# Kernel tuning notes

Measured on AMD Instinct MI355X. Metric: run time of the kernel, lower is better.

The kernel has to match this reference:

```python
import jax, jax.numpy as jnp
import numpy as np
import math

ALPHA = 1.0
EPS = 1e-8
PI = math.pi


def setup_inputs() -> dict:
    key = jax.random.key(0)
    k1, k2 = jax.random.split(key)
    B, L, P = 32, 8, 1024
    pred_keypoints = jax.random.normal(k1, (B, L, P, 2), dtype=jnp.float32)
    gt_keypoints = jax.random.normal(k2, (B, L, P, 2), dtype=jnp.float32)
    return {"pred_keypoints": pred_keypoints, "gt_keypoints": gt_keypoints}


def _segments(pts):
    """pts: [..., P, 2] -> (dl [..., S, 2], mid [..., S, 2]) with S = P-1.
    Faithful to torch: tangent = diff/sqrt(|diff|^2+eps), dl = tangent*|diff| (norm w/o eps)."""
    diff = pts[..., 1:, :] - pts[..., :-1, :]
    sumsq = jnp.sum(diff * diff, axis=-1)
    seg_len = jnp.sqrt(sumsq)                       # torch.norm(p2-p1)
    scale = seg_len / jnp.sqrt(sumsq + EPS)          # |dl| factor vs raw diff
    dl = diff * scale[..., None]
    mid = 0.5 * (pts[..., 1:, :] + pts[..., :-1, :])
    return dl, mid


def _self_energy(dl, mid):
    """dl, mid: [B, L, S, 2] -> per-lane self energy [B, L]."""
    S = dl.shape[-2]
    line = jnp.sum(jnp.linalg.norm(dl, axis=-1), axis=-1) / (8.0 * PI)
    dots = jnp.einsum('blid,bljd->blij', dl, dl)                 # [B,L,S,S]
    r = jnp.linalg.norm(mid[..., None, :, :] - mid[..., :, None, :], axis=-1) + EPS
    mask = jnp.triu(jnp.ones((S, S), dtype=bool), k=1)           # i < j pairs only
    pair = jnp.sum(jnp.where(mask, dots / (8.0 * PI * r), 0.0), axis=(-1, -2))
    return line + pair


def _interaction_energy(dl_p, mid_p, dl_g, mid_g):
    """-> per-lane interaction energy [B, L] (note dot(dl1, -dl2) in torch)."""
    dots = jnp.einsum('blid,bljd->blij', dl_p, dl_g)             # [B,L,Sp,Sg]
    r = jnp.linalg.norm(mid_g[..., None, :, :] - mid_p[..., :, None, :], axis=-1) + EPS
    return jnp.sum(-dots / (4.0 * PI * r), axis=(-1, -2))


def reference(pred_keypoints, gt_keypoints):
    B = pred_keypoints.shape[0]
    dl_p, mid_p = _segments(pred_keypoints)
    dl_g, mid_g = _segments(gt_keypoints)
    e_self_p = _self_energy(dl_p, mid_p)
    e_self_g = _self_energy(dl_g, mid_g)
    e_int = _interaction_energy(dl_p, mid_p, dl_g, mid_g)
    lane_loss = e_self_p + e_self_g - 2.0 * ALPHA * e_int        # [B, L]
    return jnp.sum(lane_loss) / B
```

## Files before the change

kernel.cpp:

```cpp
#include <hip/hip_runtime.h>
#include <math.h>

constexpr int B = 32;
constexpr int P = 1024;
constexpr int S = 1023;
constexpr float EPS = 1e-8f;

#define INV8PI 0.039788735772973836
#define INV2PI 0.15915494309189535

typedef float f32x4 __attribute__((ext_vector_type(4)));

__device__ const unsigned char UMT[36] = {
    0,0,0,0,0,0,0,0,0,0,
    1,1,1,1,1,1,1,1,1,1,
    2,2,2,2,2,2,2,2,2,2,2,2,2,2,2,2};
__device__ const unsigned char URB[36] = {
    0,0,0,0,1,1,1,2,2,3,
    0,0,0,0,1,1,1,2,2,3,
    0,0,0,0,1,1,1,1,2,2,2,2,3,3,3,3};
__device__ const unsigned char UCB[36] = {
    0,1,2,3,1,2,3,2,3,3,
    0,1,2,3,1,2,3,2,3,3,
    0,1,2,3,0,1,2,3,0,1,2,3,0,1,2,3};

__device__ __forceinline__ float4 make_seg(const float2* __restrict__ pts, int i) {
    float2 a = pts[i];
    float2 b = pts[i + 1];
    float dx = b.x - a.x, dy = b.y - a.y;
    float s2 = dx * dx + dy * dy;
    float scale = sqrtf(s2) / sqrtf(s2 + EPS);
    float4 r;
    r.x = dx * scale;
    r.y = dy * scale;
    r.z = 0.5f * (a.x + b.x);
    r.w = 0.5f * (a.y + b.y);
    return r;
}

__global__ __launch_bounds__(256, 4) void
pair_kernel(const float* __restrict__ pred, const float* __restrict__ gt,
            double* __restrict__ acc) {
    __shared__ float sA[2][4][1024];
    __shared__ double wsum[8];

    const int lane = blockIdx.y;
    const int ublk = blockIdx.x;
    const int tid  = threadIdx.x;
    const int wv   = tid >> 6;
    const int l    = tid & 63;

    const float2* pp = (const float2*)pred + (size_t)lane * P;
    const float2* pg = (const float2*)gt   + (size_t)lane * P;

    for (int j = tid; j < S; j += 256) {
        float4 s = make_seg(pp, j);
        sA[0][0][j] = s.x; sA[0][1][j] = s.y; sA[0][2][j] = s.z; sA[0][3][j] = s.w;
        float4 t = make_seg(pg, j);
        sA[1][0][j] = t.x; sA[1][1][j] = t.y; sA[1][2][j] = t.z; sA[1][3][j] = t.w;
    }
    if (tid == 0) {
        sA[0][0][S] = 0.f; sA[0][1][S] = 0.f; sA[0][2][S] = 0.f; sA[0][3][S] = 0.f;
        sA[1][0][S] = 0.f; sA[1][1][S] = 0.f; sA[1][2][S] = 0.f; sA[1][3][S] = 0.f;
    }
    __syncthreads();

    double acc_self = 0.0, acc_int = 0.0;

    if (ublk == 0) {
        float lf = 0.f;
        for (int j = tid; j < S; j += 256) {
            lf += sqrtf(sA[0][0][j] * sA[0][0][j] + sA[0][1][j] * sA[0][1][j]);
            lf += sqrtf(sA[1][0][j] * sA[1][0][j] + sA[1][1][j] * sA[1][1][j]);
        }
        acc_self += (double)lf;
    }

    for (int t = 0; t < 3; ++t) {
        const int u  = 12 * ublk + wv + 4 * t;
        const int mt = UMT[u], rb = URB[u], cb = UCB[u];
        const int rm = (mt == 1) ? 1 : 0;
        const int cm = (mt == 0) ? 0 : 1;

        const int rq = rb * 64 + l;
        f32x4 rx4 = ((const f32x4*)sA[rm][0])[rq];
        f32x4 ry4 = ((const f32x4*)sA[rm][1])[rq];
        f32x4 ru4 = ((const f32x4*)sA[rm][2])[rq];
        f32x4 rv4 = ((const f32x4*)sA[rm][3])[rq];
        const float rx[4] = {rx4.x, rx4.y, rx4.z, rx4.w};
        const float ry[4] = {ry4.x, ry4.y, ry4.z, ry4.w};
        const float ru[4] = {ru4.x, ru4.y, ru4.z, ru4.w};
        const float rv[4] = {rv4.x, rv4.y, rv4.z, rv4.w};

        const f32x4* qx = (const f32x4*)sA[cm][0];
        const f32x4* qy = (const f32x4*)sA[cm][1];
        const f32x4* qu = (const f32x4*)sA[cm][2];
        const f32x4* qv = (const f32x4*)sA[cm][3];

        f32x4 a[4] = {{0,0,0,0},{0,0,0,0},{0,0,0,0},{0,0,0,0}};
        const int q0 = cb * 64;
        const int i0 = rb * 256 + 4 * l;
        const bool masked = (mt < 2) && (rb == cb);

        if (!masked) {
#pragma unroll 2
            for (int q = q0; q < q0 + 64; ++q) {
                f32x4 cx = qx[q], cy = qy[q], cu = qu[q], cv = qv[q];
#pragma unroll
                for (int k = 0; k < 4; ++k) {
                    f32x4 rdx = cu - ru[k];
                    f32x4 rdy = cv - rv[k];
                    f32x4 d2  = rdx * rdx + (rdy * rdy + (f32x4)1e-30f);
                    f32x4 dot = rx[k] * cx + ry[k] * cy;
                    f32x4 rs;
                    rs.x = __builtin_amdgcn_rsqf(d2.x);
                    rs.y = __builtin_amdgcn_rsqf(d2.y);
                    rs.z = __builtin_amdgcn_rsqf(d2.z);
                    rs.w = __builtin_amdgcn_rsqf(d2.w);
                    a[k] += dot * rs;
                }
            }
        } else {
#pragma unroll 2
            for (int q = q0; q < q0 + 64; ++q) {
                f32x4 cx = qx[q], cy = qy[q], cu = qu[q], cv = qv[q];
                const int jb = 4 * q;
#pragma unroll
                for (int k = 0; k < 4; ++k) {
                    f32x4 rdx = cu - ru[k];
                    f32x4 rdy = cv - rv[k];
                    f32x4 d2  = rdx * rdx + (rdy * rdy + (f32x4)1e-30f);
                    f32x4 dot = rx[k] * cx + ry[k] * cy;
                    f32x4 rs;
                    rs.x = __builtin_amdgcn_rsqf(d2.x);
                    rs.y = __builtin_amdgcn_rsqf(d2.y);
                    rs.z = __builtin_amdgcn_rsqf(d2.z);
                    rs.w = __builtin_amdgcn_rsqf(d2.w);
                    f32x4 tv = dot * rs;
                    const int ik = i0 + k;
                    tv.x = (jb + 0 > ik) ? tv.x : 0.f;
                    tv.y = (jb + 1 > ik) ? tv.y : 0.f;
                    tv.z = (jb + 2 > ik) ? tv.z : 0.f;
                    tv.w = (jb + 3 > ik) ? tv.w : 0.f;
                    a[k] += tv;
                }
            }
        }

        double su = 0.0;
#pragma unroll
        for (int k = 0; k < 4; ++k)
            su += (double)a[k].x + (double)a[k].y + (double)a[k].z + (double)a[k].w;
        if (mt == 2) acc_int += su; else acc_self += su;
    }

    for (int off = 32; off; off >>= 1) {
        acc_self += __shfl_down(acc_self, off, 64);
        acc_int  += __shfl_down(acc_int,  off, 64);
    }
    if (l == 0) { wsum[wv] = acc_self; wsum[4 + wv] = acc_int; }
    __syncthreads();
    if (tid == 0) {
        double ts = wsum[0] + wsum[1] + wsum[2] + wsum[3];
        double ti = wsum[4] + wsum[5] + wsum[6] + wsum[7];
        atomicAdd(acc, ts * INV8PI + ti * INV2PI);
    }
}

__global__ void finalize_kernel(const double* __restrict__ acc, float* __restrict__ out) {
    out[0] = (float)(acc[0] / (double)B);
}

extern "C" void kernel_launch(void* const* d_in, const int* in_sizes, int n_in,
                              void* d_out, int out_size, void* d_ws, size_t ws_size,
                              hipStream_t stream) {
    const float* pred = (const float*)d_in[0];
    const float* gt   = (const float*)d_in[1];
    double* acc = (double*)d_ws;

    hipMemsetAsync(d_ws, 0, sizeof(double), stream);

    dim3 grid(3, 256);
    pair_kernel<<<grid, dim3(256), 0, stream>>>(pred, gt, acc);
    finalize_kernel<<<1, 1, 0, stream>>>(acc, (float*)d_out);
}
```

Baseline: 188.2 us.

## Split pair work into per-wave 256x32 panels across a much larger grid

Replaces the 3-block-per-lane schedule, where each wave processed three 256x256 tiles from a fully staged LDS copy, with a 72-block-per-lane grid. Each wave now handles one 256x32 panel and builds its own row and column segments from global memory. This aims to raise occupancy and load balance and to shrink wasted work on diagonal tiles. In exchange, segments are recomputed redundantly and the number of global double atomics grows greatly.

```diff
diff --git a/kernel.cpp b/kernel.cpp
--- a/kernel.cpp
+++ b/kernel.cpp
@@ -10,19 +10,6 @@
 #define INV2PI 0.15915494309189535
 
 typedef float f32x4 __attribute__((ext_vector_type(4)));
-
-__device__ const unsigned char UMT[36] = {
-    0,0,0,0,0,0,0,0,0,0,
-    1,1,1,1,1,1,1,1,1,1,
-    2,2,2,2,2,2,2,2,2,2,2,2,2,2,2,2};
-__device__ const unsigned char URB[36] = {
-    0,0,0,0,1,1,1,2,2,3,
-    0,0,0,0,1,1,1,2,2,3,
-    0,0,0,0,1,1,1,1,2,2,2,2,3,3,3,3};
-__device__ const unsigned char UCB[36] = {
-    0,1,2,3,1,2,3,2,3,3,
-    0,1,2,3,1,2,3,2,3,3,
-    0,1,2,3,0,1,2,3,0,1,2,3,0,1,2,3};
 
 __device__ __forceinline__ float4 make_seg(const float2* __restrict__ pts, int i) {
     float2 a = pts[i];
@@ -38,133 +25,121 @@
     return r;
 }
 
-__global__ __launch_bounds__(256, 4) void
+__global__ __launch_bounds__(256, 8) void
 pair_kernel(const float* __restrict__ pred, const float* __restrict__ gt,
             double* __restrict__ acc) {
-    __shared__ float sA[2][4][1024];
-    __shared__ double wsum[8];
+    __shared__ __align__(16) float pan[4][4][32];
+    __shared__ double wsum[4];
 
-    const int lane = blockIdx.y;
-    const int ublk = blockIdx.x;
-    const int tid  = threadIdx.x;
-    const int wv   = tid >> 6;
-    const int l    = tid & 63;
+    const int plane = blockIdx.y;
+    const int tid   = threadIdx.x;
+    const int wv    = tid >> 6;
+    const int l     = tid & 63;
+    const int s     = blockIdx.x * 4 + wv;
 
-    const float2* pp = (const float2*)pred + (size_t)lane * P;
-    const float2* pg = (const float2*)gt   + (size_t)lane * P;
+    int mt, rb, cs;
+    if (s < 160) {
+        mt = (s < 80) ? 0 : 1;
+        const int u = (s < 80) ? s : s - 80;
+        if      (u < 32) { rb = 0; cs = u; }
+        else if (u < 56) { rb = 1; cs = u - 32 + 8; }
+        else if (u < 72) { rb = 2; cs = u - 56 + 16; }
+        else             { rb = 3; cs = u - 72 + 24; }
+    } else {
+        mt = 2;
+        const int u = s - 160;
+        rb = u >> 5; cs = u & 31;
+    }
 
-    for (int j = tid; j < S; j += 256) {
-        float4 s = make_seg(pp, j);
-        sA[0][0][j] = s.x; sA[0][1][j] = s.y; sA[0][2][j] = s.z; sA[0][3][j] = s.w;
-        float4 t = make_seg(pg, j);
-        sA[1][0][j] = t.x; sA[1][1][j] = t.y; sA[1][2][j] = t.z; sA[1][3][j] = t.w;
+    const float2* rowpts = (const float2*)(mt == 1 ? gt : pred) + (size_t)plane * P;
+    const float2* colpts = (const float2*)(mt == 0 ? pred : gt) + (size_t)plane * P;
+
+    double accd = 0.0;
+
+    if (l < 32) {
+        const int j = cs * 32 + l;
+        float4 sg = {0.f, 0.f, 0.f, 0.f};
+        if (j < S) sg = make_seg(colpts, j);
+        pan[wv][0][l] = sg.x; pan[wv][1][l] = sg.y;
+        pan[wv][2][l] = sg.z; pan[wv][3][l] = sg.w;
+        if (mt < 2 && rb == 0)
+            accd += (double)sqrtf(sg.x * sg.x + sg.y * sg.y) * INV8PI;
     }
-    if (tid == 0) {
-        sA[0][0][S] = 0.f; sA[0][1][S] = 0.f; sA[0][2][S] = 0.f; sA[0][3][S] = 0.f;
-        sA[1][0][S] = 0.f; sA[1][1][S] = 0.f; sA[1][2][S] = 0.f; sA[1][3][S] = 0.f;
+
+    const int i0 = rb * 256 + 4 * l;
+    float rx[4], ry[4], ru[4], rv[4];
+#pragma unroll
+    for (int k = 0; k < 4; ++k) {
+        float4 r = {0.f, 0.f, 0.f, 0.f};
+        if (i0 + k < S) r = make_seg(rowpts, i0 + k);
+        rx[k] = r.x; ry[k] = r.y; ru[k] = r.z; rv[k] = r.w;
     }
     __syncthreads();
 
-    double acc_self = 0.0, acc_int = 0.0;
+    const f32x4* qx = (const f32x4*)pan[wv][0];
+    const f32x4* qy = (const f32x4*)pan[wv][1];
+    const f32x4* qu = (const f32x4*)pan[wv][2];
+    const f32x4* qv = (const f32x4*)pan[wv][3];
 
-    if (ublk == 0) {
-        float lf = 0.f;
-        for (int j = tid; j < S; j += 256) {
-            lf += sqrtf(sA[0][0][j] * sA[0][0][j] + sA[0][1][j] * sA[0][1][j]);
-            lf += sqrtf(sA[1][0][j] * sA[1][0][j] + sA[1][1][j] * sA[1][1][j]);
+    f32x4 a[4] = {{0,0,0,0},{0,0,0,0},{0,0,0,0},{0,0,0,0}};
+    const bool masked = (mt < 2) && ((cs >> 3) == rb);
+
+    if (!masked) {
+#pragma unroll
+        for (int q = 0; q < 8; ++q) {
+            f32x4 cx = qx[q], cy = qy[q], cu = qu[q], cv = qv[q];
+#pragma unroll
+            for (int k = 0; k < 4; ++k) {
+                f32x4 rdx = cu - ru[k];
+                f32x4 rdy = cv - rv[k];
+                f32x4 d2  = rdx * rdx + (rdy * rdy + (f32x4)1e-30f);
+                f32x4 dot = rx[k] * cx + ry[k] * cy;
+                f32x4 rs;
+                rs.x = __builtin_amdgcn_rsqf(d2.x);
+                rs.y = __builtin_amdgcn_rsqf(d2.y);
+                rs.z = __builtin_amdgcn_rsqf(d2.z);
+                rs.w = __builtin_amdgcn_rsqf(d2.w);
+                a[k] += dot * rs;
+            }
         }
-        acc_self += (double)lf;
+    } else {
+#pragma unroll
+        for (int q = 0; q < 8; ++q) {
+            f32x4 cx = qx[q], cy = qy[q], cu = qu[q], cv = qv[q];
+            const int jb = cs * 32 + 4 * q;
+#pragma unroll
+            for (int k = 0; k < 4; ++k) {
+                f32x4 rdx = cu - ru[k];
+                f32x4 rdy = cv - rv[k];
+                f32x4 d2  = rdx * rdx + (rdy * rdy + (f32x4)1e-30f);
+                f32x4 dot = rx[k] * cx + ry[k] * cy;
+                f32x4 rs;
+                rs.x = __builtin_amdgcn_rsqf(d2.x);
+                rs.y = __builtin_amdgcn_rsqf(d2.y);
+                rs.z = __builtin_amdgcn_rsqf(d2.z);
+                rs.w = __builtin_amdgcn_rsqf(d2.w);
+                f32x4 tv = dot * rs;
+                const int ik = i0 + k;
+                tv.x = (jb + 0 > ik) ? tv.x : 0.f;
+                tv.y = (jb + 1 > ik) ? tv.y : 0.f;
+                tv.z = (jb + 2 > ik) ? tv.z : 0.f;
+                tv.w = (jb + 3 > ik) ? tv.w : 0.f;
+                a[k] += tv;
+            }
+        }
     }
 
-    for (int t = 0; t < 3; ++t) {
-        const int u  = 12 * ublk + wv + 4 * t;
-        const int mt = UMT[u], rb = URB[u], cb = UCB[u];
-        const int rm = (mt == 1) ? 1 : 0;
-        const int cm = (mt == 0) ? 0 : 1;
+    double su = 0.0;
+#pragma unroll
+    for (int k = 0; k < 4; ++k)
+        su += (double)a[k].x + (double)a[k].y + (double)a[k].z + (double)a[k].w;
+    accd += su * ((mt == 2) ? INV2PI : INV8PI);
 
-        const int rq = rb * 64 + l;
-        f32x4 rx4 = ((const f32x4*)sA[rm][0])[rq];
-        f32x4 ry4 = ((const f32x4*)sA[rm][1])[rq];
-        f32x4 ru4 = ((const f32x4*)sA[rm][2])[rq];
-        f32x4 rv4 = ((const f32x4*)sA[rm][3])[rq];
-        const float rx[4] = {rx4.x, rx4.y, rx4.z, rx4.w};
-        const float ry[4] = {ry4.x, ry4.y, ry4.z, ry4.w};
-        const float ru[4] = {ru4.x, ru4.y, ru4.z, ru4.w};
-        const float rv[4] = {rv4.x, rv4.y, rv4.z, rv4.w};
-
-        const f32x4* qx = (const f32x4*)sA[cm][0];
-        const f32x4* qy = (const f32x4*)sA[cm][1];
-        const f32x4* qu = (const f32x4*)sA[cm][2];
-        const f32x4* qv = (const f32x4*)sA[cm][3];
-
-        f32x4 a[4] = {{0,0,0,0},{0,0,0,0},{0,0,0,0},{0,0,0,0}};
-        const int q0 = cb * 64;
-        const int i0 = rb * 256 + 4 * l;
-        const bool masked = (mt < 2) && (rb == cb);
-
-        if (!masked) {
-#pragma unroll 2
-            for (int q = q0; q < q0 + 64; ++q) {
-                f32x4 cx = qx[q], cy = qy[q], cu = qu[q], cv = qv[q];
-#pragma unroll
-                for (int k = 0; k < 4; ++k) {
-                    f32x4 rdx = cu - ru[k];
-                    f32x4 rdy = cv - rv[k];
-                    f32x4 d2  = rdx * rdx + (rdy * rdy + (f32x4)1e-30f);
-                    f32x4 dot = rx[k] * cx + ry[k] * cy;
-                    f32x4 rs;
-                    rs.x = __builtin_amdgcn_rsqf(d2.x);
-                    rs.y = __builtin_amdgcn_rsqf(d2.y);
-                    rs.z = __builtin_amdgcn_rsqf(d2.z);
-                    rs.w = __builtin_amdgcn_rsqf(d2.w);
-                    a[k] += dot * rs;
-                }
-            }
-        } else {
-#pragma unroll 2
-            for (int q = q0; q < q0 + 64; ++q) {
-                f32x4 cx = qx[q], cy = qy[q], cu = qu[q], cv = qv[q];
-                const int jb = 4 * q;
-#pragma unroll
-                for (int k = 0; k < 4; ++k) {
-                    f32x4 rdx = cu - ru[k];
-                    f32x4 rdy = cv - rv[k];
-                    f32x4 d2  = rdx * rdx + (rdy * rdy + (f32x4)1e-30f);
-                    f32x4 dot = rx[k] * cx + ry[k] * cy;
-                    f32x4 rs;
-                    rs.x = __builtin_amdgcn_rsqf(d2.x);
-                    rs.y = __builtin_amdgcn_rsqf(d2.y);
-                    rs.z = __builtin_amdgcn_rsqf(d2.z);
-                    rs.w = __builtin_amdgcn_rsqf(d2.w);
-                    f32x4 tv = dot * rs;
-                    const int ik = i0 + k;
-                    tv.x = (jb + 0 > ik) ? tv.x : 0.f;
-                    tv.y = (jb + 1 > ik) ? tv.y : 0.f;
-                    tv.z = (jb + 2 > ik) ? tv.z : 0.f;
-                    tv.w = (jb + 3 > ik) ? tv.w : 0.f;
-                    a[k] += tv;
-                }
-            }
-        }
-
-        double su = 0.0;
-#pragma unroll
-        for (int k = 0; k < 4; ++k)
-            su += (double)a[k].x + (double)a[k].y + (double)a[k].z + (double)a[k].w;
-        if (mt == 2) acc_int += su; else acc_self += su;
-    }
-
-    for (int off = 32; off; off >>= 1) {
-        acc_self += __shfl_down(acc_self, off, 64);
-        acc_int  += __shfl_down(acc_int,  off, 64);
-    }
-    if (l == 0) { wsum[wv] = acc_self; wsum[4 + wv] = acc_int; }
+    for (int off = 32; off; off >>= 1) accd += __shfl_down(accd, off, 64);
+    if (l == 0) wsum[wv] = accd;
     __syncthreads();
-    if (tid == 0) {
-        double ts = wsum[0] + wsum[1] + wsum[2] + wsum[3];
-        double ti = wsum[4] + wsum[5] + wsum[6] + wsum[7];
-        atomicAdd(acc, ts * INV8PI + ti * INV2PI);
-    }
+    if (tid == 0)
+        atomicAdd(acc, wsum[0] + wsum[1] + wsum[2] + wsum[3]);
 }
 
 __global__ void finalize_kernel(const double* __restrict__ acc, float* __restrict__ out) {
@@ -180,7 +155,7 @@
 
     hipMemsetAsync(d_ws, 0, sizeof(double), stream);
 
-    dim3 grid(3, 256);
+    dim3 grid(72, 256);
     pair_kernel<<<grid, dim3(256), 0, stream>>>(pred, gt, acc);
     finalize_kernel<<<1, 1, 0, stream>>>(acc, (float*)d_out);
 }
```

Measured after the change: 311.1 us. 65.3% more time.
